# Kernel optimization log

Hardware: AMD Instinct MI355X
Metric: run time of the kernel (lower is better)

The kernel has to match this reference:

```python
import jax, jax.numpy as jnp
import numpy as np

PALETTE = 256

def setup_inputs() -> dict:
    key = jax.random.key(0)
    k1, k2, k3, k4 = jax.random.split(key, 4)
    input = jax.random.normal(k1, (32, 256, 56, 56), dtype=jnp.float32)
    weight_idx = jax.random.randint(k2, (256, 256, 3, 3), 0, PALETTE, dtype=jnp.int32)
    lookup_table = jax.random.normal(k3, (PALETTE,), dtype=jnp.float32)
    bias = jax.random.normal(k4, (256,), dtype=jnp.float32)
    return {"input": input, "weight_idx": weight_idx,
            "lookup_table": lookup_table, "bias": bias}

def reference(input, weight_idx, lookup_table, bias):
    # Dequantize: gather palette values per weight index -> full conv weights [O,I,kH,kW]
    full_weights = lookup_table[weight_idx]
    # conv2d, stride=1, padding=1, dilation=1, groups=1, NCHW/OIHW layout
    out = jax.lax.conv_general_dilated(
        input, full_weights,
        window_strides=(1, 1),
        padding=((1, 1), (1, 1)),
        rhs_dilation=(1, 1),
        feature_group_count=1,
        dimension_numbers=("NCHW", "OIHW", "NCHW"),
    )
    return out + bias[None, :, None, None]
```

## Files before the change

### kernel.cpp

```cpp
#include <hip/hip_runtime.h>
#include <stdint.h>

#define NIMG   32
#define CCH    256
#define WDIM   56
#define HW     3136
#define MTOT   (NIMG*HW)
#define KCTOT  36
#define BK     64

typedef __attribute__((ext_vector_type(8))) short    bf16x8;
typedef __attribute__((ext_vector_type(4))) float    f32x4;
typedef __attribute__((ext_vector_type(4))) uint32_t u32x4;

typedef __attribute__((address_space(1))) const uint8_t* as1cp;
typedef __attribute__((address_space(3))) uint8_t*       as3p;

__global__ __launch_bounds__(256) void dequant_weights(
    const int* __restrict__ widx, const float* __restrict__ lut,
    uint16_t* __restrict__ Bw) {
  int idx = blockIdx.x * 256 + threadIdx.x;
  int co  = idx / (KCTOT * BK);
  int r   = idx - co * (KCTOT * BK);
  int kc  = r >> 6;
  int cil = r & 63;
  int cc  = kc / 9;
  int tap = kc - cc * 9;
  int ci  = cc * 64 + cil;
  int wv  = widx[(co * CCH + ci) * 9 + tap];
  uint32_t b  = __float_as_uint(lut[wv]);
  uint32_t rn = (b + 0x7fffu + ((b >> 16) & 1u)) >> 16;
  Bw[idx] = (uint16_t)rn;
}

__global__ __launch_bounds__(256, 2) void conv_mfma(
    const float* __restrict__ in, const uint16_t* __restrict__ Bw,
    const float* __restrict__ bias, float* __restrict__ out) {

  __shared__ __align__(16) uint16_t A_lds[257 * 72];
  __shared__ __align__(16) uint16_t B_lds[2 * 128 * 64];

  const int t    = threadIdx.x;
  const int lane = t & 63;
  const int wv   = t >> 6;
  const int wm   = wv & 1;
  const int wn   = wv >> 1;
  const int lrow = lane & 15;
  const int kgrp = lane >> 4;

  const int m0  = blockIdx.x * 128;
  const int co0 = blockIdx.y * 128;

  const int b_row8 = lane >> 3;
  const int b_g    = lane & 7;

#pragma unroll
  for (int c = 0; c < 4; ++c) {
    const int co_l = wv * 32 + c * 8 + b_row8;
    const int ck   = b_g ^ (co_l & 7);
    const uint8_t* gsrc = (const uint8_t*)(Bw + ((size_t)(co0 + co_l) * KCTOT + 0) * BK) + ck * 16;
    as3p ldst = (as3p)((uint8_t*)B_lds + (wv * 32 + c * 8) * 128);
    __builtin_amdgcn_global_load_lds((as1cp)gsrc, ldst, 16, 0, 0);
  }

  if (t < 9) *(u32x4*)((uint8_t*)A_lds + 256 * 144 + t * 16) = (u32x4){0u, 0u, 0u, 0u};

  const int st_r   = t & 31;
  const int st_grp = t >> 5;

  int hh[4], ww[4], arb[4];
#pragma unroll
  for (int mi = 0; mi < 4; ++mi) {
    const int m = m0 + wm * 64 + mi * 16 + lrow;
    const int n = m / HW;
    const int s = m - n * HW;
    hh[mi] = s / WDIM;
    ww[mi] = s - hh[mi] * WDIM;
    arb[mi] = (wm * 64 + mi * 16 + lrow + 58) * 144 + kgrp * 16;
  }
  const int zoff = 256 * 144 + kgrp * 16;

  f32x4 acc[4][4];
#pragma unroll
  for (int i = 0; i < 4; ++i)
#pragma unroll
    for (int j = 0; j < 4; ++j)
      acc[i][j] = (f32x4){0.f, 0.f, 0.f, 0.f};

#pragma unroll 1
  for (int cc = 0; cc < 4; ++cc) {
#pragma unroll
    for (int i = 0; i < 8; ++i) {
      const int r = st_r + 32 * i;
      long g = (long)m0 + r - 58;
      g = g < 0 ? 0 : (g >= MTOT ? (MTOT - 1) : g);
      const int n = (int)((unsigned long)g / HW);
      const int s = (int)(g - (long)n * HW);
      const float* p = in + (size_t)n * (CCH * HW) + (size_t)(cc * 64 + st_grp * 8) * HW + s;
      u32x4 pk;
#pragma unroll
      for (int jj = 0; jj < 4; ++jj) {
        const uint32_t b0 = __float_as_uint(p[(size_t)(2 * jj) * HW]);
        const uint32_t b1 = __float_as_uint(p[(size_t)(2 * jj + 1) * HW]);
        pk[jj] = (b0 >> 16) | (b1 & 0xffff0000u);
      }
      *(u32x4*)((uint8_t*)A_lds + r * 144 + st_grp * 16) = pk;
    }
    asm volatile("s_waitcnt lgkmcnt(0)" ::: "memory");
    __builtin_amdgcn_sched_barrier(0);
    __builtin_amdgcn_s_barrier();
    __builtin_amdgcn_sched_barrier(0);

    const int scc = (cc & 1) << 14;

#pragma unroll
    for (int tap = 0; tap < 9; ++tap) {
      const int kc    = cc * 9 + tap;
      const int rdoff = (tap & 1) ? (scc ^ 16384) : scc;
      const int wroff = rdoff ^ 16384;
      const int kc_next = (tap < 8 || cc < 3) ? kc + 1 : kc;

#pragma unroll
      for (int c = 0; c < 4; ++c) {
        const int co_l = wv * 32 + c * 8 + b_row8;
        const int ck   = b_g ^ (co_l & 7);
        const uint8_t* gsrc =
            (const uint8_t*)(Bw + ((size_t)(co0 + co_l) * KCTOT + kc_next) * BK) + ck * 16;
        as3p ldst = (as3p)((uint8_t*)B_lds + wroff + (wv * 32 + c * 8) * 128);
        __builtin_amdgcn_global_load_lds((as1cp)gsrc, ldst, 16, 0, 0);
      }
      __builtin_amdgcn_sched_barrier(0);
      asm volatile("s_waitcnt vmcnt(4)" ::: "memory");
      __builtin_amdgcn_sched_barrier(0);
      __builtin_amdgcn_s_barrier();
      __builtin_amdgcn_sched_barrier(0);

      const int kh = tap / 3;
      const int dh = kh - 1;
      const int dw = (tap - kh * 3) - 1;
      const int d  = dh * WDIM + dw;

      bf16x8 af[2][4], bfb[2][4];
#pragma unroll
      for (int mi = 0; mi < 4; ++mi) {
        const bool valid = (((unsigned)(hh[mi] + dh)) < 56u) & (((unsigned)(ww[mi] + dw)) < 56u);
        const int ad = valid ? (arb[mi] + d * 144) : zoff;
        af[0][mi] = *(const bf16x8*)((const uint8_t*)A_lds + ad);
        af[1][mi] = *(const bf16x8*)((const uint8_t*)A_lds + ad + 64);
      }
#pragma unroll
      for (int ks = 0; ks < 2; ++ks)
#pragma unroll
        for (int ni = 0; ni < 4; ++ni) {
          const int nrow = wn * 64 + ni * 16 + lrow;
          const int gran = ((ks * 4 + kgrp) ^ (lrow & 7)) * 16;
          bfb[ks][ni] = *(const bf16x8*)((const uint8_t*)B_lds + rdoff + nrow * 128 + gran);
        }

      __builtin_amdgcn_s_setprio(1);
#pragma unroll
      for (int mi = 0; mi < 4; ++mi)
#pragma unroll
        for (int ni = 0; ni < 4; ++ni)
          acc[mi][ni] = __builtin_amdgcn_mfma_f32_16x16x32_bf16(
              af[0][mi], bfb[0][ni], acc[mi][ni], 0, 0, 0);
#pragma unroll
      for (int mi = 0; mi < 4; ++mi)
#pragma unroll
        for (int ni = 0; ni < 4; ++ni)
          acc[mi][ni] = __builtin_amdgcn_mfma_f32_16x16x32_bf16(
              af[1][mi], bfb[1][ni], acc[mi][ni], 0, 0, 0);
      __builtin_amdgcn_s_setprio(0);

      __builtin_amdgcn_sched_barrier(0);
      __builtin_amdgcn_s_barrier();
      __builtin_amdgcn_sched_barrier(0);
    }
  }

  float bv[4];
#pragma unroll
  for (int ni = 0; ni < 4; ++ni)
    bv[ni] = bias[co0 + wn * 64 + ni * 16 + lrow];

#pragma unroll
  for (int mi = 0; mi < 4; ++mi) {
#pragma unroll
    for (int r = 0; r < 4; ++r) {
      const int mrow = m0 + wm * 64 + mi * 16 + kgrp * 4 + r;
      const int ni_img = mrow / HW;
      const int ss = mrow - ni_img * HW;
      float* ob = out + (size_t)ni_img * (CCH * HW) + ss;
#pragma unroll
      for (int ni = 0; ni < 4; ++ni) {
        const int co = co0 + wn * 64 + ni * 16 + lrow;
        ob[(size_t)co * HW] = acc[mi][ni][r] + bv[ni];
      }
    }
  }
}

extern "C" void kernel_launch(void* const* d_in, const int* in_sizes, int n_in,
                              void* d_out, int out_size, void* d_ws, size_t ws_size,
                              hipStream_t stream) {
  const float* in   = (const float*)d_in[0];
  const int*   widx = (const int*)d_in[1];
  const float* lut  = (const float*)d_in[2];
  const float* bias = (const float*)d_in[3];
  float* out = (float*)d_out;
  uint16_t* Bw = (uint16_t*)d_ws;

  dequant_weights<<<dim3(589824 / 256), dim3(256), 0, stream>>>(widx, lut, Bw);
  conv_mfma<<<dim3(MTOT / 128, CCH / 128), dim3(256), 0, stream>>>(in, Bw, bias, out);
}
```

Baseline: 366.4 us.

## Double block to 512 threads with 256-row M tile and XOR-swizzled A tile

Each block now has 8 waves covering 256 output pixels instead of 128, so every B-weight tile staged in LDS is reused across twice as many rows and the halo overhead is amortized. The A tile drops its padded 144-byte row stride in favor of a 128-byte stride with an XOR swizzle to avoid bank conflicts, and a dedicated zero row handles out-of-bounds taps. The B pipeline now waits on vmcnt(0) before a single barrier per tap, and LDS fragment loads are split into two half-K phases to cut register pressure. Launch bounds ask for 4 waves per SIMD, which may force register spills, and the larger LDS footprint may limit how many blocks fit per CU.

```diff
diff --git a/kernel.cpp b/kernel.cpp
--- a/kernel.cpp
+++ b/kernel.cpp
@@ -33,42 +33,37 @@
   Bw[idx] = (uint16_t)rn;
 }
 
-__global__ __launch_bounds__(256, 2) void conv_mfma(
+__global__ __launch_bounds__(512, 4) void conv_mfma(
     const float* __restrict__ in, const uint16_t* __restrict__ Bw,
     const float* __restrict__ bias, float* __restrict__ out) {
 
-  __shared__ __align__(16) uint16_t A_lds[257 * 72];
+  __shared__ __align__(16) uint16_t A_lds[372 * 64];
   __shared__ __align__(16) uint16_t B_lds[2 * 128 * 64];
 
   const int t    = threadIdx.x;
   const int lane = t & 63;
   const int wv   = t >> 6;
-  const int wm   = wv & 1;
-  const int wn   = wv >> 1;
+  const int wm   = wv & 3;
+  const int wn   = wv >> 2;
   const int lrow = lane & 15;
   const int kgrp = lane >> 4;
 
-  const int m0  = blockIdx.x * 128;
+  const int m0  = blockIdx.x * 256;
   const int co0 = blockIdx.y * 128;
 
   const int b_row8 = lane >> 3;
   const int b_g    = lane & 7;
 
 #pragma unroll
-  for (int c = 0; c < 4; ++c) {
-    const int co_l = wv * 32 + c * 8 + b_row8;
+  for (int c = 0; c < 2; ++c) {
+    const int co_l = wv * 16 + c * 8 + b_row8;
     const int ck   = b_g ^ (co_l & 7);
-    const uint8_t* gsrc = (const uint8_t*)(Bw + ((size_t)(co0 + co_l) * KCTOT + 0) * BK) + ck * 16;
-    as3p ldst = (as3p)((uint8_t*)B_lds + (wv * 32 + c * 8) * 128);
+    const uint8_t* gsrc = (const uint8_t*)(Bw + ((size_t)(co0 + co_l) * KCTOT) * BK) + ck * 16;
+    as3p ldst = (as3p)((uint8_t*)B_lds + (wv * 16 + c * 8) * 128);
     __builtin_amdgcn_global_load_lds((as1cp)gsrc, ldst, 16, 0, 0);
   }
 
-  if (t < 9) *(u32x4*)((uint8_t*)A_lds + 256 * 144 + t * 16) = (u32x4){0u, 0u, 0u, 0u};
-
-  const int st_r   = t & 31;
-  const int st_grp = t >> 5;
-
-  int hh[4], ww[4], arb[4];
+  int hh[4], ww[4], rbase[4];
 #pragma unroll
   for (int mi = 0; mi < 4; ++mi) {
     const int m = m0 + wm * 64 + mi * 16 + lrow;
@@ -76,9 +71,8 @@
     const int s = m - n * HW;
     hh[mi] = s / WDIM;
     ww[mi] = s - hh[mi] * WDIM;
-    arb[mi] = (wm * 64 + mi * 16 + lrow + 58) * 144 + kgrp * 16;
-  }
-  const int zoff = 256 * 144 + kgrp * 16;
+    rbase[mi] = wm * 64 + mi * 16 + lrow + 58;
+  }
 
   f32x4 acc[4][4];
 #pragma unroll
@@ -89,22 +83,32 @@
 
 #pragma unroll 1
   for (int cc = 0; cc < 4; ++cc) {
-#pragma unroll
-    for (int i = 0; i < 8; ++i) {
-      const int r = st_r + 32 * i;
-      long g = (long)m0 + r - 58;
-      g = g < 0 ? 0 : (g >= MTOT ? (MTOT - 1) : g);
-      const int n = (int)((unsigned long)g / HW);
-      const int s = (int)(g - (long)n * HW);
-      const float* p = in + (size_t)n * (CCH * HW) + (size_t)(cc * 64 + st_grp * 8) * HW + s;
-      u32x4 pk;
-#pragma unroll
-      for (int jj = 0; jj < 4; ++jj) {
-        const uint32_t b0 = __float_as_uint(p[(size_t)(2 * jj) * HW]);
-        const uint32_t b1 = __float_as_uint(p[(size_t)(2 * jj + 1) * HW]);
-        pk[jj] = (b0 >> 16) | (b1 & 0xffff0000u);
-      }
-      *(u32x4*)((uint8_t*)A_lds + r * 144 + st_grp * 16) = pk;
+    if (cc) {
+      __builtin_amdgcn_sched_barrier(0);
+      __builtin_amdgcn_s_barrier();
+      __builtin_amdgcn_sched_barrier(0);
+    }
+
+#pragma unroll
+    for (int i = 0; i < 6; ++i) {
+      const int r = lane + 64 * i;
+      if (r < 372) {
+        u32x4 pk = (u32x4){0u, 0u, 0u, 0u};
+        if (r != 371) {
+          long g = (long)m0 + r - 58;
+          g = g < 0 ? 0 : (g >= MTOT ? (MTOT - 1) : g);
+          const int n = (int)((unsigned long)g / HW);
+          const int s = (int)(g - (long)n * HW);
+          const float* p = in + (size_t)n * (CCH * HW) + (size_t)(cc * 64 + wv * 8) * HW + s;
+#pragma unroll
+          for (int jj = 0; jj < 4; ++jj) {
+            const uint32_t b0 = __float_as_uint(p[(size_t)(2 * jj) * HW]);
+            const uint32_t b1 = __float_as_uint(p[(size_t)(2 * jj + 1) * HW]);
+            pk[jj] = (b0 >> 16) | (b1 & 0xffff0000u);
+          }
+        }
+        *(u32x4*)((uint8_t*)A_lds + r * 128 + ((wv ^ (r & 7)) << 4)) = pk;
+      }
     }
     asm volatile("s_waitcnt lgkmcnt(0)" ::: "memory");
     __builtin_amdgcn_sched_barrier(0);
@@ -115,66 +119,78 @@
 
 #pragma unroll
     for (int tap = 0; tap < 9; ++tap) {
-      const int kc    = cc * 9 + tap;
-      const int rdoff = (tap & 1) ? (scc ^ 16384) : scc;
-      const int wroff = rdoff ^ 16384;
-      const int kc_next = (tap < 8 || cc < 3) ? kc + 1 : kc;
-
-#pragma unroll
-      for (int c = 0; c < 4; ++c) {
-        const int co_l = wv * 32 + c * 8 + b_row8;
+      const int kc      = cc * 9 + tap;
+      const int rdoff   = scc ^ ((tap & 1) << 14);
+      const int wroff   = rdoff ^ 16384;
+      const int kc_next = (tap == 8 && cc == 3) ? 35 : kc + 1;
+
+      asm volatile("s_waitcnt vmcnt(0)" ::: "memory");
+      __builtin_amdgcn_sched_barrier(0);
+      __builtin_amdgcn_s_barrier();
+      __builtin_amdgcn_sched_barrier(0);
+
+#pragma unroll
+      for (int c = 0; c < 2; ++c) {
+        const int co_l = wv * 16 + c * 8 + b_row8;
         const int ck   = b_g ^ (co_l & 7);
         const uint8_t* gsrc =
             (const uint8_t*)(Bw + ((size_t)(co0 + co_l) * KCTOT + kc_next) * BK) + ck * 16;
-        as3p ldst = (as3p)((uint8_t*)B_lds + wroff + (wv * 32 + c * 8) * 128);
+        as3p ldst = (as3p)((uint8_t*)B_lds + wroff + (wv * 16 + c * 8) * 128);
         __builtin_amdgcn_global_load_lds((as1cp)gsrc, ldst, 16, 0, 0);
       }
-      __builtin_amdgcn_sched_barrier(0);
-      asm volatile("s_waitcnt vmcnt(4)" ::: "memory");
-      __builtin_amdgcn_sched_barrier(0);
-      __builtin_amdgcn_s_barrier();
-      __builtin_amdgcn_sched_barrier(0);
 
       const int kh = tap / 3;
       const int dh = kh - 1;
       const int dw = (tap - kh * 3) - 1;
       const int d  = dh * WDIM + dw;
 
-      bf16x8 af[2][4], bfb[2][4];
+      bf16x8 a0[4], b0[4];
 #pragma unroll
       for (int mi = 0; mi < 4; ++mi) {
         const bool valid = (((unsigned)(hh[mi] + dh)) < 56u) & (((unsigned)(ww[mi] + dw)) < 56u);
-        const int ad = valid ? (arb[mi] + d * 144) : zoff;
-        af[0][mi] = *(const bf16x8*)((const uint8_t*)A_lds + ad);
-        af[1][mi] = *(const bf16x8*)((const uint8_t*)A_lds + ad + 64);
-      }
-#pragma unroll
-      for (int ks = 0; ks < 2; ++ks)
-#pragma unroll
-        for (int ni = 0; ni < 4; ++ni) {
-          const int nrow = wn * 64 + ni * 16 + lrow;
-          const int gran = ((ks * 4 + kgrp) ^ (lrow & 7)) * 16;
-          bfb[ks][ni] = *(const bf16x8*)((const uint8_t*)B_lds + rdoff + nrow * 128 + gran);
-        }
-
+        const int row = rbase[mi] + d;
+        const int ad  = valid ? (row * 128 + ((kgrp ^ (row & 7)) << 4))
+                              : (371 * 128 + (kgrp << 4));
+        a0[mi] = *(const bf16x8*)((const uint8_t*)A_lds + ad);
+      }
+#pragma unroll
+      for (int ni = 0; ni < 4; ++ni) {
+        const int nrow = wn * 64 + ni * 16 + lrow;
+        b0[ni] = *(const bf16x8*)((const uint8_t*)B_lds + rdoff + nrow * 128 +
+                                  ((kgrp ^ (lrow & 7)) << 4));
+      }
       __builtin_amdgcn_s_setprio(1);
 #pragma unroll
       for (int mi = 0; mi < 4; ++mi)
 #pragma unroll
         for (int ni = 0; ni < 4; ++ni)
           acc[mi][ni] = __builtin_amdgcn_mfma_f32_16x16x32_bf16(
-              af[0][mi], bfb[0][ni], acc[mi][ni], 0, 0, 0);
+              a0[mi], b0[ni], acc[mi][ni], 0, 0, 0);
+      __builtin_amdgcn_s_setprio(0);
+
+      bf16x8 a1[4], b1[4];
+#pragma unroll
+      for (int mi = 0; mi < 4; ++mi) {
+        const bool valid = (((unsigned)(hh[mi] + dh)) < 56u) & (((unsigned)(ww[mi] + dw)) < 56u);
+        const int row = rbase[mi] + d;
+        const int ad  = valid ? (row * 128 + (((4 + kgrp) ^ (row & 7)) << 4))
+                              : (371 * 128 + ((4 + kgrp) << 4));
+        a1[mi] = *(const bf16x8*)((const uint8_t*)A_lds + ad);
+      }
+#pragma unroll
+      for (int ni = 0; ni < 4; ++ni) {
+        const int nrow = wn * 64 + ni * 16 + lrow;
+        b1[ni] = *(const bf16x8*)((const uint8_t*)B_lds + rdoff + nrow * 128 +
+                                  (((4 + kgrp) ^ (lrow & 7)) << 4));
+      }
+      __builtin_amdgcn_s_setprio(1);
 #pragma unroll
       for (int mi = 0; mi < 4; ++mi)
 #pragma unroll
         for (int ni = 0; ni < 4; ++ni)
           acc[mi][ni] = __builtin_amdgcn_mfma_f32_16x16x32_bf16(
-              af[1][mi], bfb[1][ni], acc[mi][ni], 0, 0, 0);
+              a1[mi], b1[ni], acc[mi][ni], 0, 0, 0);
       __builtin_amdgcn_s_setprio(0);
-
-      __builtin_amdgcn_sched_barrier(0);
-      __builtin_amdgcn_s_barrier();
-      __builtin_amdgcn_sched_barrier(0);
     }
   }
 
@@ -211,5 +227,5 @@
   uint16_t* Bw = (uint16_t*)d_ws;
 
   dequant_weights<<<dim3(589824 / 256), dim3(256), 0, stream>>>(widx, lut, Bw);
-  conv_mfma<<<dim3(MTOT / 128, CCH / 128), dim3(256), 0, stream>>>(in, Bw, bias, out);
+  conv_mfma<<<dim3(MTOT / 256, CCH / 128), dim3(512), 0, stream>>>(in, Bw, bias, out);
 }
```

New measurement: 566.6 us. 1.55x slower.

## Re-layout weights and LDS tiles k-group-major, reduce barriers, remap block order

Applied to the files above, without the earlier changes.

The dequantized weight buffer is stored k-group-major ([kc][g][co][8]), so B tiles load contiguously and LDS reads need no XOR swizzle. The A tile in LDS moves to a per-8-channel-group layout with 244 rows instead of a padded 144-byte row stride. The per-tap sync becomes a single vmcnt(0) wait plus barrier before issuing the next prefetch, replacing the vmcnt(4) wait and the trailing barrier. Block IDs are remapped so blocks scheduled together share output-channel tiles and neighbouring M tiles. The new LDS layouts may cause bank conflicts, and the full vmcnt(0) wait can expose global-load latency.

```diff
diff --git a/kernel.cpp b/kernel.cpp
--- a/kernel.cpp
+++ b/kernel.cpp
@@ -7,7 +7,8 @@
 #define HW     3136
 #define MTOT   (NIMG*HW)
 #define KCTOT  36
-#define BK     64
+#define AROWS  244
+#define AGB    (AROWS*16)
 
 typedef __attribute__((ext_vector_type(8))) short    bf16x8;
 typedef __attribute__((ext_vector_type(4))) float    f32x4;
@@ -18,27 +19,28 @@
 
 __global__ __launch_bounds__(256) void dequant_weights(
     const int* __restrict__ widx, const float* __restrict__ lut,
-    uint16_t* __restrict__ Bw) {
+    uint16_t* __restrict__ Bw2) {
   int idx = blockIdx.x * 256 + threadIdx.x;
-  int co  = idx / (KCTOT * BK);
-  int r   = idx - co * (KCTOT * BK);
-  int kc  = r >> 6;
-  int cil = r & 63;
+  int e   = idx & 7;
+  int co  = (idx >> 3) & 255;
+  int gk  = idx >> 11;
+  int kc  = gk >> 3;
+  int g   = gk & 7;
   int cc  = kc / 9;
   int tap = kc - cc * 9;
-  int ci  = cc * 64 + cil;
+  int ci  = cc * 64 + g * 8 + e;
   int wv  = widx[(co * CCH + ci) * 9 + tap];
   uint32_t b  = __float_as_uint(lut[wv]);
   uint32_t rn = (b + 0x7fffu + ((b >> 16) & 1u)) >> 16;
-  Bw[idx] = (uint16_t)rn;
+  Bw2[idx] = (uint16_t)rn;
 }
 
 __global__ __launch_bounds__(256, 2) void conv_mfma(
-    const float* __restrict__ in, const uint16_t* __restrict__ Bw,
+    const float* __restrict__ in, const uint16_t* __restrict__ Bw2,
     const float* __restrict__ bias, float* __restrict__ out) {
 
-  __shared__ __align__(16) uint16_t A_lds[257 * 72];
-  __shared__ __align__(16) uint16_t B_lds[2 * 128 * 64];
+  __shared__ __align__(16) uint16_t A_lds[8 * AROWS * 8];
+  __shared__ __align__(16) uint16_t B_lds[2 * 8 * 128 * 8];
 
   const int t    = threadIdx.x;
   const int lane = t & 63;
@@ -48,27 +50,23 @@
   const int lrow = lane & 15;
   const int kgrp = lane >> 4;
 
-  const int m0  = blockIdx.x * 128;
-  const int co0 = blockIdx.y * 128;
-
-  const int b_row8 = lane >> 3;
-  const int b_g    = lane & 7;
+  const int bid = blockIdx.x + gridDim.x * blockIdx.y;
+  const int nid = (bid & 7) * 196 + (bid >> 3);
+  const int m0  = (nid % 784) * 128;
+  const int co0 = (nid / 784) * 128;
 
 #pragma unroll
   for (int c = 0; c < 4; ++c) {
-    const int co_l = wv * 32 + c * 8 + b_row8;
-    const int ck   = b_g ^ (co_l & 7);
-    const uint8_t* gsrc = (const uint8_t*)(Bw + ((size_t)(co0 + co_l) * KCTOT + 0) * BK) + ck * 16;
-    as3p ldst = (as3p)((uint8_t*)B_lds + (wv * 32 + c * 8) * 128);
-    __builtin_amdgcn_global_load_lds((as1cp)gsrc, ldst, 16, 0, 0);
-  }
-
-  if (t < 9) *(u32x4*)((uint8_t*)A_lds + 256 * 144 + t * 16) = (u32x4){0u, 0u, 0u, 0u};
-
-  const int st_r   = t & 31;
-  const int st_grp = t >> 5;
-
-  int hh[4], ww[4], arb[4];
+    const int gid = c * 256 + t;
+    const uint8_t* gsrc = (const uint8_t*)Bw2 +
+        ((size_t)(gid >> 7) << 12) + (size_t)(co0 + (gid & 127)) * 16;
+    as3p ldst = (as3p)((uint8_t*)B_lds + (c * 256 + wv * 64) * 16);
+    __builtin_amdgcn_global_load_lds(gsrc, ldst, 16, 0, 0);
+  }
+
+  if (t < 8) *(u32x4*)((uint8_t*)A_lds + t * AGB + 243 * 16) = (u32x4){0u, 0u, 0u, 0u};
+
+  int hh[4], ww[4], rbase[4];
 #pragma unroll
   for (int mi = 0; mi < 4; ++mi) {
     const int m = m0 + wm * 64 + mi * 16 + lrow;
@@ -76,9 +74,8 @@
     const int s = m - n * HW;
     hh[mi] = s / WDIM;
     ww[mi] = s - hh[mi] * WDIM;
-    arb[mi] = (wm * 64 + mi * 16 + lrow + 58) * 144 + kgrp * 16;
-  }
-  const int zoff = 256 * 144 + kgrp * 16;
+    rbase[mi] = wm * 64 + mi * 16 + lrow + 58;
+  }
 
   f32x4 acc[4][4];
 #pragma unroll
@@ -89,51 +86,57 @@
 
 #pragma unroll 1
   for (int cc = 0; cc < 4; ++cc) {
+    if (cc) {
+      __builtin_amdgcn_sched_barrier(0);
+      __builtin_amdgcn_s_barrier();
+      __builtin_amdgcn_sched_barrier(0);
+    }
+
 #pragma unroll
     for (int i = 0; i < 8; ++i) {
-      const int r = st_r + 32 * i;
-      long g = (long)m0 + r - 58;
-      g = g < 0 ? 0 : (g >= MTOT ? (MTOT - 1) : g);
-      const int n = (int)((unsigned long)g / HW);
-      const int s = (int)(g - (long)n * HW);
-      const float* p = in + (size_t)n * (CCH * HW) + (size_t)(cc * 64 + st_grp * 8) * HW + s;
-      u32x4 pk;
-#pragma unroll
-      for (int jj = 0; jj < 4; ++jj) {
-        const uint32_t b0 = __float_as_uint(p[(size_t)(2 * jj) * HW]);
-        const uint32_t b1 = __float_as_uint(p[(size_t)(2 * jj + 1) * HW]);
-        pk[jj] = (b0 >> 16) | (b1 & 0xffff0000u);
-      }
-      *(u32x4*)((uint8_t*)A_lds + r * 144 + st_grp * 16) = pk;
+      const int r = (t & 31) + 32 * i;
+      if (r <= 242) {
+        const int g = t >> 5;
+        long gm = (long)m0 + r - 58;
+        gm = gm < 0 ? 0 : (gm >= MTOT ? (MTOT - 1) : gm);
+        const int n = (int)((unsigned long)gm / HW);
+        const int s = (int)(gm - (long)n * HW);
+        const float* p = in + (size_t)n * (CCH * HW) + (size_t)(cc * 64 + g * 8) * HW + s;
+        u32x4 pk;
+#pragma unroll
+        for (int jj = 0; jj < 4; ++jj) {
+          const uint32_t b0 = __float_as_uint(p[(size_t)(2 * jj) * HW]);
+          const uint32_t b1 = __float_as_uint(p[(size_t)(2 * jj + 1) * HW]);
+          pk[jj] = (b0 >> 16) | (b1 & 0xffff0000u);
+        }
+        *(u32x4*)((uint8_t*)A_lds + g * AGB + r * 16) = pk;
+      }
     }
     asm volatile("s_waitcnt lgkmcnt(0)" ::: "memory");
     __builtin_amdgcn_sched_barrier(0);
     __builtin_amdgcn_s_barrier();
     __builtin_amdgcn_sched_barrier(0);
 
-    const int scc = (cc & 1) << 14;
-
 #pragma unroll
     for (int tap = 0; tap < 9; ++tap) {
       const int kc    = cc * 9 + tap;
-      const int rdoff = (tap & 1) ? (scc ^ 16384) : scc;
-      const int wroff = rdoff ^ 16384;
-      const int kc_next = (tap < 8 || cc < 3) ? kc + 1 : kc;
+      const int rdoff = (kc & 1) << 14;
+      const int wroff = rdoff ^ (1 << 14);
+      const int kcn   = (kc < 35) ? kc + 1 : 35;
+
+      asm volatile("s_waitcnt vmcnt(0)" ::: "memory");
+      __builtin_amdgcn_sched_barrier(0);
+      __builtin_amdgcn_s_barrier();
+      __builtin_amdgcn_sched_barrier(0);
 
 #pragma unroll
       for (int c = 0; c < 4; ++c) {
-        const int co_l = wv * 32 + c * 8 + b_row8;
-        const int ck   = b_g ^ (co_l & 7);
-        const uint8_t* gsrc =
-            (const uint8_t*)(Bw + ((size_t)(co0 + co_l) * KCTOT + kc_next) * BK) + ck * 16;
-        as3p ldst = (as3p)((uint8_t*)B_lds + wroff + (wv * 32 + c * 8) * 128);
-        __builtin_amdgcn_global_load_lds((as1cp)gsrc, ldst, 16, 0, 0);
-      }
-      __builtin_amdgcn_sched_barrier(0);
-      asm volatile("s_waitcnt vmcnt(4)" ::: "memory");
-      __builtin_amdgcn_sched_barrier(0);
-      __builtin_amdgcn_s_barrier();
-      __builtin_amdgcn_sched_barrier(0);
+        const int gid = c * 256 + t;
+        const uint8_t* gsrc = (const uint8_t*)Bw2 + (size_t)kcn * 32768 +
+            ((size_t)(gid >> 7) << 12) + (size_t)(co0 + (gid & 127)) * 16;
+        as3p ldst = (as3p)((uint8_t*)B_lds + wroff + (c * 256 + wv * 64) * 16);
+        __builtin_amdgcn_global_load_lds(gsrc, ldst, 16, 0, 0);
+      }
 
       const int kh = tap / 3;
       const int dh = kh - 1;
@@ -144,37 +147,30 @@
 #pragma unroll
       for (int mi = 0; mi < 4; ++mi) {
         const bool valid = (((unsigned)(hh[mi] + dh)) < 56u) & (((unsigned)(ww[mi] + dw)) < 56u);
-        const int ad = valid ? (arb[mi] + d * 144) : zoff;
-        af[0][mi] = *(const bf16x8*)((const uint8_t*)A_lds + ad);
-        af[1][mi] = *(const bf16x8*)((const uint8_t*)A_lds + ad + 64);
+        const int r = valid ? (rbase[mi] + d) : 243;
+#pragma unroll
+        for (int ks = 0; ks < 2; ++ks)
+          af[ks][mi] = *(const bf16x8*)((const uint8_t*)A_lds + (ks * 4 + kgrp) * AGB + r * 16);
       }
 #pragma unroll
       for (int ks = 0; ks < 2; ++ks)
 #pragma unroll
         for (int ni = 0; ni < 4; ++ni) {
-          const int nrow = wn * 64 + ni * 16 + lrow;
-          const int gran = ((ks * 4 + kgrp) ^ (lrow & 7)) * 16;
-          bfb[ks][ni] = *(const bf16x8*)((const uint8_t*)B_lds + rdoff + nrow * 128 + gran);
+          const int col = wn * 64 + ni * 16 + lrow;
+          bfb[ks][ni] = *(const bf16x8*)((const uint8_t*)B_lds + rdoff +
+                                         (ks * 4 + kgrp) * 2048 + col * 16);
         }
 
       __builtin_amdgcn_s_setprio(1);
 #pragma unroll
-      for (int mi = 0; mi < 4; ++mi)
-#pragma unroll
-        for (int ni = 0; ni < 4; ++ni)
-          acc[mi][ni] = __builtin_amdgcn_mfma_f32_16x16x32_bf16(
-              af[0][mi], bfb[0][ni], acc[mi][ni], 0, 0, 0);
-#pragma unroll
-      for (int mi = 0; mi < 4; ++mi)
-#pragma unroll
-        for (int ni = 0; ni < 4; ++ni)
-          acc[mi][ni] = __builtin_amdgcn_mfma_f32_16x16x32_bf16(
-              af[1][mi], bfb[1][ni], acc[mi][ni], 0, 0, 0);
+      for (int ks = 0; ks < 2; ++ks)
+#pragma unroll
+        for (int mi = 0; mi < 4; ++mi)
+#pragma unroll
+          for (int ni = 0; ni < 4; ++ni)
+            acc[mi][ni] = __builtin_amdgcn_mfma_f32_16x16x32_bf16(
+                af[ks][mi], bfb[ks][ni], acc[mi][ni], 0, 0, 0);
       __builtin_amdgcn_s_setprio(0);
-
-      __builtin_amdgcn_sched_barrier(0);
-      __builtin_amdgcn_s_barrier();
-      __builtin_amdgcn_sched_barrier(0);
     }
   }
 
@@ -208,8 +204,8 @@
   const float* lut  = (const float*)d_in[2];
   const float* bias = (const float*)d_in[3];
   float* out = (float*)d_out;
-  uint16_t* Bw = (uint16_t*)d_ws;
-
-  dequant_weights<<<dim3(589824 / 256), dim3(256), 0, stream>>>(widx, lut, Bw);
-  conv_mfma<<<dim3(MTOT / 128, CCH / 128), dim3(256), 0, stream>>>(in, Bw, bias, out);
+  uint16_t* Bw2 = (uint16_t*)d_ws;
+
+  dequant_weights<<<dim3(589824 / 256), dim3(256), 0, stream>>>(widx, lut, Bw2);
+  conv_mfma<<<dim3(MTOT / 128, CCH / 128), dim3(256), 0, stream>>>(in, Bw2, bias, out);
 }
```

After: 342.6 us. -6.5%, faster.
